# Optimization experiments

Measured on AMD Instinct MI355X. Metric: run time of the kernel, lower is better.

## Reference

```python
import jax, jax.numpy as jnp
import numpy as np

LOG_2PI = float(np.log(2.0 * np.pi))
MASK_SCORE = -1.0e15


def setup_inputs() -> dict:
    key = jax.random.key(0)
    k1, k2, k3, k4 = jax.random.split(key, 4)
    B, H, D, T = 32, 600, 512, 2400
    encoder_outputs = jax.random.normal(k1, (B, H, D), dtype=jnp.float32)
    # per-phoneme durations in frames (float, as the torch code casts via cumsum().float())
    durations = jax.random.randint(k2, (B, H), 0, 8).astype(jnp.float32)
    # per-phoneme Gaussian variances; keep strictly positive for log(vars)
    vars_ = jax.random.uniform(k3, (B, H), dtype=jnp.float32) * 0.9 + 0.1
    input_lengths = jax.random.randint(k4, (B,), 1, H, dtype=jnp.int32)
    return {
        "encoder_outputs": encoder_outputs,
        "durations": durations,
        "vars": vars_,
        "input_lengths": input_lengths,
        "frame_length": T,
    }


def reference(encoder_outputs, durations, vars, input_lengths, frame_length):
    # encoder_outputs: [B, H, D]; durations, vars: [B, H]; input_lengths: [B]
    B, H, D = encoder_outputs.shape
    # Gaussian centers: cumulative duration minus half the phoneme's own duration
    c = jnp.cumsum(durations, axis=1) - 0.5 * durations            # [B, H]
    t = jnp.arange(frame_length, dtype=jnp.float32)                 # [T]
    # log N(t; c, vars): [B, H, T]
    diff = t[None, None, :] - c[:, :, None]
    w_t = -0.5 * (LOG_2PI + jnp.log(vars)[:, :, None] + diff * diff / vars[:, :, None])
    # mask out padded phoneme positions (h >= input_length)
    pad_mask = jnp.arange(H)[None, :] >= input_lengths[:, None]     # [B, H]
    w_t = jnp.where(pad_mask[:, :, None], MASK_SCORE, w_t)
    # softmax over the phoneme (hidden) axis
    w_t = jax.nn.softmax(w_t, axis=1)                                # [B, H, T]
    # upsample: [B, T, H] @ [B, H, D] -> [B, T, D]
    return jnp.einsum("bht,bhd->btd", w_t, encoder_outputs)
```

## Files before the change

### kernel.cpp

```cpp
#include <hip/hip_runtime.h>
#include <hip/hip_bf16.h>

using f32x4   = __attribute__((ext_vector_type(4))) float;
using short8  = __attribute__((ext_vector_type(8))) short;
using short4v = __attribute__((ext_vector_type(4))) short;

#define LOG2_2PI 2.6514961294723187f
#define L2E_HALF 0.7213475204444817f
#define HP2 640

__device__ __forceinline__ short bf16bits(float x) {
  unsigned u = __builtin_bit_cast(unsigned, x);
  u = (u + 0x7FFFu + ((u >> 16) & 1u)) >> 16;
  return (short)u;
}
__device__ __forceinline__ float bf16round(float x) {
  unsigned u = __builtin_bit_cast(unsigned, x);
  u = ((u + 0x7FFFu + ((u >> 16) & 1u)) >> 16) << 16;
  return __builtin_bit_cast(float, u);
}

__global__ void prepwin_kernel(const float* __restrict__ dur,
                               const float* __restrict__ vars,
                               const int* __restrict__ lens,
                               f32x4* __restrict__ pk, int* __restrict__ win,
                               int H, int T, int TT) {
  __shared__ float sc[HP2];
  __shared__ float sAux[8];

  const int b   = blockIdx.x;
  const int tid = threadIdx.x;
  const int L   = lens[b];

  if (tid < 64) {
    const int l = tid;
    float run = 0.f, prevD = 0.f;
    float Gmax = 0.f, qMin = 1e30f, qMax = 0.f, bMin = 1e30f, bMax = -1e30f;
    for (int h0 = 0; h0 < HP2; h0 += 64) {
      const int h = h0 + l;
      const float d = (h < H) ? dur[(size_t)b * H + h] : 0.f;
      float x = d;
#pragma unroll
      for (int off = 1; off < 64; off <<= 1) {
        float y = __shfl_up(x, off);
        if (l >= off) x += y;
      }
      float dp = __shfl_up(d, 1);
      if (l == 0) dp = prevD;
      f32x4 e = (f32x4){0.f, 0.f, -1e30f, 0.f};
      if (h < H) {
        const float v = vars[(size_t)b * H + h];
        const float q = L2E_HALF / v;
        const float bc = -0.5f * (LOG2_2PI + __builtin_amdgcn_logf(v));
        e[0] = run + x - 0.5f * d;
        e[1] = q;
        e[2] = (h < L) ? bc : -1e30f;
        if (h < L) {
          qMin = fminf(qMin, q); qMax = fmaxf(qMax, q);
          bMin = fminf(bMin, bc); bMax = fmaxf(bMax, bc);
          if (h >= 1) Gmax = fmaxf(Gmax, 0.5f * (d + dp));
        }
      }
      pk[(size_t)b * HP2 + h] = e;
      sc[h] = e[0];
      prevD = __shfl(d, 63);
      run += __shfl(x, 63);
    }
#pragma unroll
    for (int off = 1; off < 64; off <<= 1) {
      qMin = fminf(qMin, __shfl_xor(qMin, off));
      qMax = fmaxf(qMax, __shfl_xor(qMax, off));
      bMin = fminf(bMin, __shfl_xor(bMin, off));
      bMax = fmaxf(bMax, __shfl_xor(bMax, off));
      Gmax = fmaxf(Gmax, __shfl_xor(Gmax, off));
    }
    if (l == 0) {
      sAux[0] = Gmax; sAux[1] = qMin; sAux[2] = qMax; sAux[3] = bMin; sAux[4] = bMax;
    }
  }
  __syncthreads();

  const float Gmax = sAux[0], qMn = sAux[1], qMx = sAux[2];
  const float bMn  = sAux[3], bMx = sAux[4];
  const float c0 = sc[0], cL = sc[L - 1];
  for (int tile = tid; tile < TT; tile += 128) {
    const float tLo = (float)(tile * 32);
    const float tHi = (float)(min(tile * 32 + 31, T - 1));
    const float D0 = fmaxf(0.5f * Gmax, fmaxf(fmaxf(c0 - tLo, tHi - cL), 0.f));
    const float Wr = __fsqrt_rn(((bMx - bMn) + 65.f + qMx * D0 * D0) / qMn);
    int lo = 0, hi = L;
    const float thLo = tLo - Wr;
    while (lo < hi) { const int mid = (lo + hi) >> 1; if (sc[mid] < thLo) lo = mid + 1; else hi = mid; }
    int hLo = lo;
    int lo2 = hLo, hi2 = L;
    const float thHi = tHi + Wr;
    while (lo2 < hi2) { const int mid = (lo2 + hi2) >> 1; if (sc[mid] <= thHi) lo2 = mid + 1; else hi2 = mid; }
    int hHi = lo2;
    if (hHi <= hLo) { hLo = max(hLo - 1, 0); hHi = min(hLo + 2, L); }
    win[(b * TT + tile) * 2 + 0] = hLo >> 6;
    win[(b * TT + tile) * 2 + 1] = (hHi + 63) >> 6;
  }
}

__global__ void transpose_kernel(const float* __restrict__ enc,
                                 short* __restrict__ encT,
                                 const int* __restrict__ lens,
                                 int H, int D) {
  __shared__ short sT[64][66];
  const int b  = blockIdx.z;
  const int h0 = blockIdx.y * 64;
  const int d0 = blockIdx.x * 64;
  const int Lpad = (lens[b] + 63) & ~63;
  if (h0 >= Lpad) return;
  const int tid = threadIdx.x;

  const int dc = (tid & 15) * 4;
  const int hr = tid >> 4;
#pragma unroll
  for (int ps = 0; ps < 4; ++ps) {
    const int hh = hr + ps * 16;
    const int h  = h0 + hh;
    f32x4 v = (h < H) ? *(const f32x4*)&enc[((size_t)b * H + h) * D + d0 + dc]
                      : (f32x4){0.f, 0.f, 0.f, 0.f};
#pragma unroll
    for (int j = 0; j < 4; ++j) sT[dc + j][hh] = bf16bits(v[j]);
  }
  __syncthreads();

  const int tx4 = (tid & 15) * 4;
  const int ty2 = tid >> 4;
#pragma unroll
  for (int i = 0; i < 4; ++i) {
    const int d = d0 + ty2 + i * 16;
    short4v v;
#pragma unroll
    for (int j = 0; j < 4; ++j) v[j] = sT[ty2 + i * 16][tx4 + j];
    *(short4v*)&encT[((size_t)b * D + d) * HP2 + h0 + tx4] = v;
  }
}

__launch_bounds__(256, 3)
__global__ void gup_kernel(const short* __restrict__ encT,
                           const f32x4* __restrict__ pk,
                           const int* __restrict__ win,
                           float* __restrict__ out,
                           int T, int TT) {
  constexpr int D  = 512;
  constexpr int AS = 72;

  __shared__ __align__(16) float sc[HP2], sq[HP2], sb[HP2];
  __shared__ float sden[32];
  __shared__ short sA[2][32 * AS];

  const int tid   = threadIdx.x;
  const int b     = blockIdx.y;
  const int tIdx  = blockIdx.x >> 1;
  const int t0    = tIdx * 32;
  const int dbase = (blockIdx.x & 1) * 256;

  const int cLo = win[(b * TT + tIdx) * 2 + 0];
  const int cHi = win[(b * TT + tIdx) * 2 + 1];
  const int base = cLo * 64;
  const int nC   = cHi - cLo;
  const int W64  = nC * 64;

  for (int i = tid; i < W64; i += 256) {
    const f32x4 v = pk[(size_t)b * HP2 + base + i];
    sc[i] = v[0]; sq[i] = v[1]; sb[i] = v[2];
  }
  __syncthreads();

  const int tfA = tid >> 3;
  const int hs8 = tid & 7;
  const float tA = (float)(t0 + tfA);
  float mA = -1e30f;
  for (int h4 = hs8 * 4; h4 < W64; h4 += 32) {
    const f32x4 cv = *(const f32x4*)&sc[h4];
    const f32x4 qv = *(const f32x4*)&sq[h4];
    const f32x4 bv = *(const f32x4*)&sb[h4];
#pragma unroll
    for (int j = 0; j < 4; ++j) {
      const float dd = tA - cv[j];
      mA = fmaxf(mA, fmaf(-dd * dd, qv[j], bv[j]));
    }
  }
  mA = fmaxf(mA, __shfl_xor(mA, 1));
  mA = fmaxf(mA, __shfl_xor(mA, 2));
  mA = fmaxf(mA, __shfl_xor(mA, 4));

  const int lane = tid & 63;
  const int wv   = tid >> 6;
  const int l15  = lane & 15;
  const int lq   = lane >> 4;

  f32x4 acc[2][4];
#pragma unroll
  for (int i = 0; i < 2; ++i)
#pragma unroll
    for (int j = 0; j < 4; ++j) acc[i][j] = (f32x4){0.f, 0.f, 0.f, 0.f};

  const int k8 = hs8 * 8;
  float denAcc = 0.f;
  const short* bp = encT + ((size_t)b * D + dbase + wv * 64 + l15) * HP2 + base + lq * 8;

  int p = 0;
  for (int cc = 0; cc < nC; ++cc) {
    const int hb = cc * 64 + k8;
    const f32x4 cv0 = *(const f32x4*)&sc[hb];
    const f32x4 qv0 = *(const f32x4*)&sq[hb];
    const f32x4 bv0 = *(const f32x4*)&sb[hb];
    const f32x4 cv1 = *(const f32x4*)&sc[hb + 4];
    const f32x4 qv1 = *(const f32x4*)&sq[hb + 4];
    const f32x4 bv1 = *(const f32x4*)&sb[hb + 4];
    short8 w;
    float denAdd = 0.f, pmax = 0.f;
#pragma unroll
    for (int j = 0; j < 4; ++j) {
      const float dd = tA - cv0[j];
      const float pv = __builtin_amdgcn_exp2f(fmaf(-dd * dd, qv0[j], bv0[j]) - mA);
      w[j] = bf16bits(pv);
      denAdd += bf16round(pv);
      pmax = fmaxf(pmax, pv);
    }
#pragma unroll
    for (int j = 0; j < 4; ++j) {
      const float dd = tA - cv1[j];
      const float pv = __builtin_amdgcn_exp2f(fmaf(-dd * dd, qv1[j], bv1[j]) - mA);
      w[4 + j] = bf16bits(pv);
      denAdd += bf16round(pv);
      pmax = fmaxf(pmax, pv);
    }

    if (!__syncthreads_or(pmax > 1e-20f)) continue;

    denAcc += denAdd;
    *(short8*)&sA[p][tfA * AS + k8] = w;
    __syncthreads();

#pragma unroll
    for (int kh = 0; kh < 2; ++kh) {
      short8 bfv[4];
#pragma unroll
      for (int nt = 0; nt < 4; ++nt)
        bfv[nt] = *(const short8*)(bp + (size_t)nt * 16 * HP2 + cc * 64 + kh * 32);
      short8 af[2];
#pragma unroll
      for (int mt = 0; mt < 2; ++mt)
        af[mt] = *(short8*)&sA[p][(mt * 16 + l15) * AS + kh * 32 + lq * 8];
#pragma unroll
      for (int mt = 0; mt < 2; ++mt)
#pragma unroll
        for (int nt = 0; nt < 4; ++nt)
          acc[mt][nt] = __builtin_amdgcn_mfma_f32_16x16x32_bf16(bfv[nt], af[mt], acc[mt][nt], 0, 0, 0);
    }
    p ^= 1;
  }

  {
    float dsum = denAcc;
    dsum += __shfl_xor(dsum, 1);
    dsum += __shfl_xor(dsum, 2);
    dsum += __shfl_xor(dsum, 4);
    if (hs8 == 0) sden[tfA] = dsum;
  }
  __syncthreads();

#pragma unroll
  for (int mt = 0; mt < 2; ++mt) {
    const int tg = t0 + mt * 16 + l15;
    const float inv = 1.0f / sden[mt * 16 + l15];
    if (tg < T) {
#pragma unroll
      for (int nt = 0; nt < 4; ++nt) {
        f32x4 o;
#pragma unroll
        for (int i = 0; i < 4; ++i) o[i] = acc[mt][nt][i] * inv;
        *(f32x4*)&out[((size_t)b * T + tg) * D + dbase + wv * 64 + nt * 16 + lq * 4] = o;
      }
    }
  }
}

extern "C" void kernel_launch(void* const* d_in, const int* in_sizes, int n_in,
                              void* d_out, int out_size, void* d_ws, size_t ws_size,
                              hipStream_t stream) {
  const float* enc  = (const float*)d_in[0];
  const float* dur  = (const float*)d_in[1];
  const float* vars = (const float*)d_in[2];
  const int*   lens = (const int*)d_in[3];

  const int B = in_sizes[3];
  const int H = in_sizes[1] / B;
  const int D = in_sizes[0] / in_sizes[1];
  const int T = out_size / (B * D);
  const int TT = (T + 31) / 32;
  (void)n_in; (void)ws_size;

  f32x4* pk  = (f32x4*)d_ws;
  int*   wn  = (int*)(pk + (size_t)B * HP2);
  short* encT = (short*)(wn + (size_t)B * TT * 2);

  prepwin_kernel<<<B, 128, 0, stream>>>(dur, vars, lens, pk, wn, H, T, TT);

  dim3 tgrid(D / 64, HP2 / 64, B);
  transpose_kernel<<<tgrid, 256, 0, stream>>>(enc, encT, lens, H, D);

  dim3 grid(TT * 2, B);
  gup_kernel<<<grid, 256, 0, stream>>>(encT, pk, wn, (float*)d_out, T, TT);
}
```

Before: 72.20 us.

## Merge prep and transpose kernels; prefetch first B tile; drop a barrier

Folds the prepwin and transpose kernels into a single producer launch, using an extra grid row of blocks for the per-batch prefix/window work. This removes one kernel launch and lets the two independent jobs run concurrently. In the main kernel, the first chunk of encT fragments is prefetched before the shared-memory fill. The sA store is moved ahead of the syncthreads_or so the separate __syncthreads can be dropped. The prep blocks now idle most of their 256 threads, and only one of the eight x-blocks in the extra row does work.

```diff
diff --git a/kernel.cpp b/kernel.cpp
--- a/kernel.cpp
+++ b/kernel.cpp
@@ -20,99 +20,98 @@
   return __builtin_bit_cast(float, u);
 }
 
-__global__ void prepwin_kernel(const float* __restrict__ dur,
-                               const float* __restrict__ vars,
-                               const int* __restrict__ lens,
-                               f32x4* __restrict__ pk, int* __restrict__ win,
-                               int H, int T, int TT) {
+__global__ void producer_kernel(const float* __restrict__ enc,
+                                const float* __restrict__ dur,
+                                const float* __restrict__ vars,
+                                const int* __restrict__ lens,
+                                short* __restrict__ encT,
+                                f32x4* __restrict__ pk, int* __restrict__ win,
+                                int H, int D, int T, int TT) {
+  __shared__ short sT[64][66];
   __shared__ float sc[HP2];
   __shared__ float sAux[8];
 
-  const int b   = blockIdx.x;
+  const int b   = blockIdx.z;
   const int tid = threadIdx.x;
   const int L   = lens[b];
 
-  if (tid < 64) {
-    const int l = tid;
-    float run = 0.f, prevD = 0.f;
-    float Gmax = 0.f, qMin = 1e30f, qMax = 0.f, bMin = 1e30f, bMax = -1e30f;
-    for (int h0 = 0; h0 < HP2; h0 += 64) {
-      const int h = h0 + l;
-      const float d = (h < H) ? dur[(size_t)b * H + h] : 0.f;
-      float x = d;
+  if (blockIdx.y == HP2 / 64) {
+    if (blockIdx.x != 0) return;
+    if (tid < 64) {
+      const int l = tid;
+      float run = 0.f, prevD = 0.f;
+      float Gmax = 0.f, qMin = 1e30f, qMax = 0.f, bMin = 1e30f, bMax = -1e30f;
+      for (int h0 = 0; h0 < HP2; h0 += 64) {
+        const int h = h0 + l;
+        const float d = (h < H) ? dur[(size_t)b * H + h] : 0.f;
+        float x = d;
+#pragma unroll
+        for (int off = 1; off < 64; off <<= 1) {
+          float y = __shfl_up(x, off);
+          if (l >= off) x += y;
+        }
+        float dp = __shfl_up(d, 1);
+        if (l == 0) dp = prevD;
+        f32x4 e = (f32x4){0.f, 0.f, -1e30f, 0.f};
+        if (h < H) {
+          const float v = vars[(size_t)b * H + h];
+          const float q = L2E_HALF / v;
+          const float bc = -0.5f * (LOG2_2PI + __builtin_amdgcn_logf(v));
+          e[0] = run + x - 0.5f * d;
+          e[1] = q;
+          e[2] = (h < L) ? bc : -1e30f;
+          if (h < L) {
+            qMin = fminf(qMin, q); qMax = fmaxf(qMax, q);
+            bMin = fminf(bMin, bc); bMax = fmaxf(bMax, bc);
+            if (h >= 1) Gmax = fmaxf(Gmax, 0.5f * (d + dp));
+          }
+        }
+        pk[(size_t)b * HP2 + h] = e;
+        sc[h] = e[0];
+        prevD = __shfl(d, 63);
+        run += __shfl(x, 63);
+      }
 #pragma unroll
       for (int off = 1; off < 64; off <<= 1) {
-        float y = __shfl_up(x, off);
-        if (l >= off) x += y;
-      }
-      float dp = __shfl_up(d, 1);
-      if (l == 0) dp = prevD;
-      f32x4 e = (f32x4){0.f, 0.f, -1e30f, 0.f};
-      if (h < H) {
-        const float v = vars[(size_t)b * H + h];
-        const float q = L2E_HALF / v;
-        const float bc = -0.5f * (LOG2_2PI + __builtin_amdgcn_logf(v));
-        e[0] = run + x - 0.5f * d;
-        e[1] = q;
-        e[2] = (h < L) ? bc : -1e30f;
-        if (h < L) {
-          qMin = fminf(qMin, q); qMax = fmaxf(qMax, q);
-          bMin = fminf(bMin, bc); bMax = fmaxf(bMax, bc);
-          if (h >= 1) Gmax = fmaxf(Gmax, 0.5f * (d + dp));
-        }
-      }
-      pk[(size_t)b * HP2 + h] = e;
-      sc[h] = e[0];
-      prevD = __shfl(d, 63);
-      run += __shfl(x, 63);
-    }
-#pragma unroll
-    for (int off = 1; off < 64; off <<= 1) {
-      qMin = fminf(qMin, __shfl_xor(qMin, off));
-      qMax = fmaxf(qMax, __shfl_xor(qMax, off));
-      bMin = fminf(bMin, __shfl_xor(bMin, off));
-      bMax = fmaxf(bMax, __shfl_xor(bMax, off));
-      Gmax = fmaxf(Gmax, __shfl_xor(Gmax, off));
-    }
-    if (l == 0) {
-      sAux[0] = Gmax; sAux[1] = qMin; sAux[2] = qMax; sAux[3] = bMin; sAux[4] = bMax;
-    }
-  }
-  __syncthreads();
-
-  const float Gmax = sAux[0], qMn = sAux[1], qMx = sAux[2];
-  const float bMn  = sAux[3], bMx = sAux[4];
-  const float c0 = sc[0], cL = sc[L - 1];
-  for (int tile = tid; tile < TT; tile += 128) {
-    const float tLo = (float)(tile * 32);
-    const float tHi = (float)(min(tile * 32 + 31, T - 1));
-    const float D0 = fmaxf(0.5f * Gmax, fmaxf(fmaxf(c0 - tLo, tHi - cL), 0.f));
-    const float Wr = __fsqrt_rn(((bMx - bMn) + 65.f + qMx * D0 * D0) / qMn);
-    int lo = 0, hi = L;
-    const float thLo = tLo - Wr;
-    while (lo < hi) { const int mid = (lo + hi) >> 1; if (sc[mid] < thLo) lo = mid + 1; else hi = mid; }
-    int hLo = lo;
-    int lo2 = hLo, hi2 = L;
-    const float thHi = tHi + Wr;
-    while (lo2 < hi2) { const int mid = (lo2 + hi2) >> 1; if (sc[mid] <= thHi) lo2 = mid + 1; else hi2 = mid; }
-    int hHi = lo2;
-    if (hHi <= hLo) { hLo = max(hLo - 1, 0); hHi = min(hLo + 2, L); }
-    win[(b * TT + tile) * 2 + 0] = hLo >> 6;
-    win[(b * TT + tile) * 2 + 1] = (hHi + 63) >> 6;
-  }
-}
-
-__global__ void transpose_kernel(const float* __restrict__ enc,
-                                 short* __restrict__ encT,
-                                 const int* __restrict__ lens,
-                                 int H, int D) {
-  __shared__ short sT[64][66];
-  const int b  = blockIdx.z;
+        qMin = fminf(qMin, __shfl_xor(qMin, off));
+        qMax = fmaxf(qMax, __shfl_xor(qMax, off));
+        bMin = fminf(bMin, __shfl_xor(bMin, off));
+        bMax = fmaxf(bMax, __shfl_xor(bMax, off));
+        Gmax = fmaxf(Gmax, __shfl_xor(Gmax, off));
+      }
+      if (l == 0) {
+        sAux[0] = Gmax; sAux[1] = qMin; sAux[2] = qMax; sAux[3] = bMin; sAux[4] = bMax;
+      }
+    }
+    __syncthreads();
+
+    const float Gmax = sAux[0], qMn = sAux[1], qMx = sAux[2];
+    const float bMn  = sAux[3], bMx = sAux[4];
+    const float c0 = sc[0], cL = sc[L - 1];
+    for (int tile = tid; tile < TT; tile += 256) {
+      const float tLo = (float)(tile * 32);
+      const float tHi = (float)(min(tile * 32 + 31, T - 1));
+      const float D0 = fmaxf(0.5f * Gmax, fmaxf(fmaxf(c0 - tLo, tHi - cL), 0.f));
+      const float Wr = __fsqrt_rn(((bMx - bMn) + 65.f + qMx * D0 * D0) / qMn);
+      int lo = 0, hi = L;
+      const float thLo = tLo - Wr;
+      while (lo < hi) { const int mid = (lo + hi) >> 1; if (sc[mid] < thLo) lo = mid + 1; else hi = mid; }
+      int hLo = lo;
+      int lo2 = hLo, hi2 = L;
+      const float thHi = tHi + Wr;
+      while (lo2 < hi2) { const int mid = (lo2 + hi2) >> 1; if (sc[mid] <= thHi) lo2 = mid + 1; else hi2 = mid; }
+      int hHi = lo2;
+      if (hHi <= hLo) { hLo = max(hLo - 1, 0); hHi = min(hLo + 2, L); }
+      win[(b * TT + tile) * 2 + 0] = hLo >> 6;
+      win[(b * TT + tile) * 2 + 1] = (hHi + 63) >> 6;
+    }
+    return;
+  }
+
   const int h0 = blockIdx.y * 64;
   const int d0 = blockIdx.x * 64;
-  const int Lpad = (lens[b] + 63) & ~63;
+  const int Lpad = (L + 63) & ~63;
   if (h0 >= Lpad) return;
-  const int tid = threadIdx.x;
 
   const int dc = (tid & 15) * 4;
   const int hr = tid >> 4;
@@ -164,6 +163,17 @@
   const int nC   = cHi - cLo;
   const int W64  = nC * 64;
 
+  const int lane = tid & 63;
+  const int wv   = tid >> 6;
+  const int l15  = lane & 15;
+  const int lq   = lane >> 4;
+  const short* bp = encT + ((size_t)b * D + dbase + wv * 64 + l15) * HP2 + base + lq * 8;
+
+  short8 pf[4];
+#pragma unroll
+  for (int nt = 0; nt < 4; ++nt)
+    pf[nt] = *(const short8*)(bp + (size_t)nt * 16 * HP2);
+
   for (int i = tid; i < W64; i += 256) {
     const f32x4 v = pk[(size_t)b * HP2 + base + i];
     sc[i] = v[0]; sq[i] = v[1]; sb[i] = v[2];
@@ -188,11 +198,6 @@
   mA = fmaxf(mA, __shfl_xor(mA, 2));
   mA = fmaxf(mA, __shfl_xor(mA, 4));
 
-  const int lane = tid & 63;
-  const int wv   = tid >> 6;
-  const int l15  = lane & 15;
-  const int lq   = lane >> 4;
-
   f32x4 acc[2][4];
 #pragma unroll
   for (int i = 0; i < 2; ++i)
@@ -201,7 +206,6 @@
 
   const int k8 = hs8 * 8;
   float denAcc = 0.f;
-  const short* bp = encT + ((size_t)b * D + dbase + wv * 64 + l15) * HP2 + base + lq * 8;
 
   int p = 0;
   for (int cc = 0; cc < nC; ++cc) {
@@ -231,18 +235,23 @@
       pmax = fmaxf(pmax, pv);
     }
 
+    *(short8*)&sA[p][tfA * AS + k8] = w;
+
     if (!__syncthreads_or(pmax > 1e-20f)) continue;
 
     denAcc += denAdd;
-    *(short8*)&sA[p][tfA * AS + k8] = w;
-    __syncthreads();
 
 #pragma unroll
     for (int kh = 0; kh < 2; ++kh) {
       short8 bfv[4];
-#pragma unroll
-      for (int nt = 0; nt < 4; ++nt)
-        bfv[nt] = *(const short8*)(bp + (size_t)nt * 16 * HP2 + cc * 64 + kh * 32);
+      if (cc == 0 && kh == 0) {
+#pragma unroll
+        for (int nt = 0; nt < 4; ++nt) bfv[nt] = pf[nt];
+      } else {
+#pragma unroll
+        for (int nt = 0; nt < 4; ++nt)
+          bfv[nt] = *(const short8*)(bp + (size_t)nt * 16 * HP2 + cc * 64 + kh * 32);
+      }
       short8 af[2];
 #pragma unroll
       for (int mt = 0; mt < 2; ++mt)
@@ -300,10 +309,9 @@
   int*   wn  = (int*)(pk + (size_t)B * HP2);
   short* encT = (short*)(wn + (size_t)B * TT * 2);
 
-  prepwin_kernel<<<B, 128, 0, stream>>>(dur, vars, lens, pk, wn, H, T, TT);
-
-  dim3 tgrid(D / 64, HP2 / 64, B);
-  transpose_kernel<<<tgrid, 256, 0, stream>>>(enc, encT, lens, H, D);
+  dim3 pgrid(D / 64, HP2 / 64 + 1, B);
+  producer_kernel<<<pgrid, 256, 0, stream>>>(enc, dur, vars, lens, encT, pk, wn,
+                                             H, D, T, TT);
 
   dim3 grid(TT * 2, B);
   gup_kernel<<<grid, 256, 0, stream>>>(encT, pk, wn, (float*)d_out, T, TT);
```

Result: faster. 67.65 us (-6.3%).
